# Optimization experiments

Measured on AMD Instinct MI355X. Metric: run time of the kernel, lower is better.

## Reference

```python
import jax, jax.numpy as jnp
import numpy as np

B, T, FEA, H, OUT, L = 40, 20, 200, 1024, 1095, 12


def setup_inputs() -> dict:
    key = jax.random.key(0)
    ks = jax.random.split(key, 8)

    def init(k, shape, fan_in):
        return jax.random.normal(k, shape, jnp.float32) * (1.0 / np.sqrt(fan_in))

    return {
        "x": jax.random.normal(ks[0], (B, T, FEA), jnp.float32),
        "hidden": jnp.zeros((L, B, H), jnp.float32),  # initial SRU cell state c0 per layer
        "W1": init(ks[1], (FEA, H), FEA),
        "b1": jnp.zeros((H,), jnp.float32),
        "sru_W": init(ks[2], (L, H, 3 * H), H),   # per layer: [x_tilde | f-gate | r-gate]
        "sru_b": jnp.zeros((L, 2 * H), jnp.float32),  # per layer: [b_f | b_r]
        "W3": init(ks[3], (H, H), H),
        "b3": jnp.zeros((H,), jnp.float32),
        "W4": init(ks[4], (H, OUT), H),
        "b4": jnp.zeros((OUT,), jnp.float32),
    }


def _sru_layer(x, c0, W, b):
    # x: [t, b, h]; SRU (Lei et al. 2017) with use_tanh=True and highway on x
    U = jnp.einsum('tbh,hk->tbk', x, W)          # [t, b, 3h]
    x_tilde, uf, ur = jnp.split(U, 3, axis=-1)
    bf, br = jnp.split(b, 2)
    f = jax.nn.sigmoid(uf + bf)                  # forget gate
    r = jax.nn.sigmoid(ur + br)                  # reset/highway gate

    def step(c, ins):
        ft, xt = ins
        c = ft * c + (1.0 - ft) * xt
        return c, c

    c_last, cs = jax.lax.scan(step, c0, (f, x_tilde))
    h = r * jnp.tanh(cs) + (1.0 - r) * x
    return h, c_last


def reference(x, hidden, W1, b1, sru_W, sru_b, W3, b3, W4, b4):
    b, t, _ = x.shape
    # Dense_layer1 (dropout is identity at inference)
    h = jnp.dot(x.reshape(b * t, -1), W1) + b1
    h = h.reshape(b, t, H).transpose(1, 0, 2)    # [t, b, H] (time-major for SRU)
    c_finals = []
    for l in range(sru_W.shape[0]):
        h, c_l = _sru_layer(h, hidden[l], sru_W[l], sru_b[l])
        c_finals.append(c_l)
    hidden_after = jnp.stack(c_finals)           # [L, b, H]
    h = h.transpose(1, 0, 2).reshape(b * t, H)
    h = jax.nn.relu(jnp.dot(h, W3) + b3)
    out = jnp.dot(h, W4) + b4                    # [b*t, OUT]
    return out, hidden_after
```

## Files before the change

kernel.cpp:

```cpp
#include <hip/hip_runtime.h>
#include <hip/hip_bf16.h>
#include <math.h>

typedef __bf16 bf16_t;
typedef __bf16 bf16x8 __attribute__((ext_vector_type(8)));
typedef float f32x4 __attribute__((ext_vector_type(4)));
typedef unsigned short u16;

#define NB   40
#define NT   20
#define FEA  200
#define HD   1024
#define NOUT 1095
#define NL   12
#define M_ROWS 800
#define UPITCH 196

#define FBUF 36864
#define GBUF 24576

__global__ __launch_bounds__(256)
void transpose_convert(const float* __restrict__ src, bf16_t* __restrict__ dst,
                       int srcK, int srcN, int Kp, int Np)
{
    __shared__ u16 tile[64 * 66];
    const int t = threadIdx.x;
    src += (size_t)blockIdx.z * srcK * srcN;
    dst += (size_t)blockIdx.z * Np * Kp;
    const int n0 = blockIdx.x << 6, k0 = blockIdx.y << 6;
    {
        const int nl = t & 63, kb = (t >> 6) << 4;
        const int gn = n0 + nl;
        #pragma unroll
        for (int j = 0; j < 16; j++) {
            const int gk = k0 + kb + j;
            float v = (gk < srcK && gn < srcN) ? src[(size_t)gk * srcN + gn] : 0.f;
            bf16_t b = (bf16_t)v;
            tile[nl * 66 + kb + j] = *(const u16*)&b;
        }
    }
    __syncthreads();
    {
        const int nl = t >> 2, kg = (t & 3) << 4;
        const unsigned* tp = (const unsigned*)tile;
        const int dw = nl * 33 + (kg >> 1);
        uint4 v0, v1;
        v0.x = tp[dw+0]; v0.y = tp[dw+1]; v0.z = tp[dw+2]; v0.w = tp[dw+3];
        v1.x = tp[dw+4]; v1.y = tp[dw+5]; v1.z = tp[dw+6]; v1.w = tp[dw+7];
        bf16_t* dp = dst + (size_t)(n0 + nl) * Kp + k0 + kg;
        *(uint4*)dp = v0;
        *(uint4*)(dp + 8) = v1;
    }
}

__global__ __launch_bounds__(256)
void convert_pad_x(const float* __restrict__ src, bf16_t* __restrict__ dst)
{
    const int m = blockIdx.x, k = threadIdx.x;
    dst[m * 256 + k] = (bf16_t)((k < FEA) ? src[(size_t)m * FEA + k] : 0.f);
}

template<bool OUT_F32, bool RELU>
__global__ __launch_bounds__(256)
void gemm_tiled(const bf16_t* __restrict__ A, const bf16_t* __restrict__ Bt,
                const float* __restrict__ bias, void* __restrict__ C,
                int M, int Nstore, int Ks)
{
    extern __shared__ char lds[];
    const int tid = threadIdx.x;
    const int w = tid >> 6, lane = tid & 63, quad = lane >> 4, l16 = lane & 15;
    const int n0 = blockIdx.x << 6;
    const int m0 = blockIdx.y << 7;
    const int wr = w >> 1, wc = w & 1;

    const int lrow  = lane >> 3;
    const int gslot = ((lane & 7) ^ lrow) << 3;
    const bf16_t* aSrc[4];
    const bf16_t* bSrc[2];
    #pragma unroll
    for (int i = 0; i < 4; i++) {
        int r = m0 + (w * 4 + i) * 8 + lrow;
        if (r > M - 1) r = M - 1;
        aSrc[i] = A + (size_t)r * Ks + gslot;
    }
    #pragma unroll
    for (int i = 0; i < 2; i++)
        bSrc[i] = Bt + (size_t)(n0 + (w * 2 + i) * 8 + lrow) * Ks + gslot;

    f32x4 acc[4][2];
    #pragma unroll
    for (int m = 0; m < 4; m++)
        #pragma unroll
        for (int n = 0; n < 2; n++) acc[m][n] = (f32x4){0.f, 0.f, 0.f, 0.f};

    const int nkt = Ks >> 6;

    #define STAGE(kt) do {                                                     \
        const int _k0 = (kt) << 6;                                             \
        char* _b = lds + ((kt) & 3) * GBUF;                                    \
        _Pragma("unroll")                                                      \
        for (int _i = 0; _i < 4; _i++)                                         \
            __builtin_amdgcn_global_load_lds(                                  \
                (const __attribute__((address_space(1))) void*)(aSrc[_i] + _k0),\
                (__attribute__((address_space(3))) void*)(_b + (w * 4 + _i) * 1024), \
                16, 0, 0);                                                     \
        _Pragma("unroll")                                                      \
        for (int _i = 0; _i < 2; _i++)                                         \
            __builtin_amdgcn_global_load_lds(                                  \
                (const __attribute__((address_space(1))) void*)(bSrc[_i] + _k0),\
                (__attribute__((address_space(3))) void*)(_b + 16384 + (w * 2 + _i) * 1024), \
                16, 0, 0);                                                     \
    } while (0)

    STAGE(0);
    if (nkt > 1) STAGE(1);

    for (int kt = 0; kt < nkt; kt++) {
        if (kt + 2 < nkt) STAGE(kt + 2);
        const int rem = nkt - 1 - kt;
        if (rem >= 2)      asm volatile("s_waitcnt vmcnt(12)" ::: "memory");
        else if (rem == 1) asm volatile("s_waitcnt vmcnt(6)"  ::: "memory");
        else               asm volatile("s_waitcnt vmcnt(0)"  ::: "memory");
        __builtin_amdgcn_s_barrier();

        const char* ab = lds + (kt & 3) * GBUF;
        #pragma unroll
        for (int kk = 0; kk < 2; kk++) {
            const int ts = (kk << 2) + quad;
            bf16x8 a[4], b[2];
            #pragma unroll
            for (int m = 0; m < 4; m++) {
                const int r = wr * 64 + m * 16 + l16;
                a[m] = *(const bf16x8*)(ab + r * 128 + ((ts ^ (r & 7)) << 4));
            }
            #pragma unroll
            for (int n = 0; n < 2; n++) {
                const int r = wc * 32 + n * 16 + l16;
                b[n] = *(const bf16x8*)(ab + 16384 + r * 128 + ((ts ^ (r & 7)) << 4));
            }
            #pragma unroll
            for (int m = 0; m < 4; m++)
                #pragma unroll
                for (int n = 0; n < 2; n++)
                    acc[m][n] = __builtin_amdgcn_mfma_f32_16x16x32_bf16(a[m], b[n], acc[m][n], 0, 0, 0);
        }
    }
    #undef STAGE

    #pragma unroll
    for (int n = 0; n < 2; n++) {
        const int col = n0 + wc * 32 + n * 16 + l16;
        if (col >= Nstore) continue;
        const float bv = bias ? bias[col] : 0.f;
        #pragma unroll
        for (int m = 0; m < 4; m++) {
            #pragma unroll
            for (int i = 0; i < 4; i++) {
                const int mg = m0 + wr * 64 + m * 16 + quad * 4 + i;
                if (mg < M) {
                    float v = acc[m][n][i] + bv;
                    if (RELU) v = v > 0.f ? v : 0.f;
                    if (OUT_F32) ((float*)C)[(size_t)mg * Nstore + col] = v;
                    else         ((bf16_t*)C)[(size_t)mg * Nstore + col] = (bf16_t)v;
                }
            }
        }
    }
}

__global__ __launch_bounds__(256)
void sru_layer_fused(const bf16_t* __restrict__ hin, bf16_t* __restrict__ hout,
                     const bf16_t* __restrict__ Wt, const float* __restrict__ c0,
                     const float* __restrict__ bvec, float* __restrict__ cout)
{
    extern __shared__ char lds_raw[];
    const int tid = threadIdx.x;
    const int w = tid >> 6, lane = tid & 63, quad = lane >> 4, l16 = lane & 15;
    const int n0 = blockIdx.x << 6;
    const int m0 = blockIdx.y * 80;

    const int lrow  = lane >> 3;
    const int gslot = ((lane & 7) ^ lrow) << 3;

    const bf16_t* aSrc[3];
    #pragma unroll
    for (int i = 0; i < 3; i++) {
        int r = (w * 3 + i) * 8 + lrow;
        if (r > 79) r = 79;
        aSrc[i] = hin + (size_t)(m0 + r) * HD + gslot;
    }
    const bf16_t* bSrc[6];
    #pragma unroll
    for (int i = 0; i < 6; i++) {
        const int r = (w * 6 + i) * 8 + lrow;
        bSrc[i] = Wt + (size_t)((r >> 6) * HD + n0 + (r & 63)) * HD + gslot;
    }

    f32x4 acc[5][3];
    #pragma unroll
    for (int m = 0; m < 5; m++)
        #pragma unroll
        for (int n = 0; n < 3; n++) acc[m][n] = (f32x4){0.f, 0.f, 0.f, 0.f};

    #define STAGEF(kt) do {                                                    \
        const int _k0 = (kt) << 6;                                             \
        char* _b = lds_raw + ((kt) & 3) * FBUF;                                \
        _Pragma("unroll")                                                      \
        for (int _i = 0; _i < 3; _i++)                                         \
            __builtin_amdgcn_global_load_lds(                                  \
                (const __attribute__((address_space(1))) void*)(aSrc[_i] + _k0), \
                (__attribute__((address_space(3))) void*)(_b + (w * 3 + _i) * 1024), \
                16, 0, 0);                                                     \
        _Pragma("unroll")                                                      \
        for (int _i = 0; _i < 6; _i++)                                         \
            __builtin_amdgcn_global_load_lds(                                  \
                (const __attribute__((address_space(1))) void*)(bSrc[_i] + _k0), \
                (__attribute__((address_space(3))) void*)(_b + 12288 + (w * 6 + _i) * 1024), \
                16, 0, 0);                                                     \
    } while (0)

    STAGEF(0);
    STAGEF(1);

    for (int kt = 0; kt < 16; kt++) {
        if (kt + 2 < 16) STAGEF(kt + 2);
        const int rem = 15 - kt;
        if (rem >= 2)      asm volatile("s_waitcnt vmcnt(18)" ::: "memory");
        else if (rem == 1) asm volatile("s_waitcnt vmcnt(9)"  ::: "memory");
        else               asm volatile("s_waitcnt vmcnt(0)"  ::: "memory");
        __builtin_amdgcn_s_barrier();

        const char* ab = lds_raw + (kt & 3) * FBUF;
        const char* bb = ab + 12288;
        #pragma unroll
        for (int kk = 0; kk < 2; kk++) {
            const int ts = (kk << 2) + quad;
            bf16x8 a[5], b[3];
            #pragma unroll
            for (int m = 0; m < 5; m++) {
                const int r = m * 16 + l16;
                a[m] = *(const bf16x8*)(ab + r * 128 + ((ts ^ (r & 7)) << 4));
            }
            #pragma unroll
            for (int n = 0; n < 3; n++) {
                const int r = (w * 3 + n) * 16 + l16;
                b[n] = *(const bf16x8*)(bb + r * 128 + ((ts ^ (r & 7)) << 4));
            }
            #pragma unroll
            for (int m = 0; m < 5; m++)
                #pragma unroll
                for (int n = 0; n < 3; n++)
                    acc[m][n] = __builtin_amdgcn_mfma_f32_16x16x32_bf16(a[m], b[n], acc[m][n], 0, 0, 0);
        }
    }
    #undef STAGEF

    float* Ul = (float*)lds_raw;
    #pragma unroll
    for (int m = 0; m < 5; m++)
        #pragma unroll
        for (int n = 0; n < 3; n++) {
            const int col = (w * 3 + n) * 16 + l16;
            #pragma unroll
            for (int i = 0; i < 4; i++)
                Ul[(m * 16 + quad * 4 + i) * UPITCH + col] = acc[m][n][i];
        }
    __syncthreads();

    const int bl = tid >> 6, nn = tid & 63, bg = blockIdx.y * 4 + bl;
    float c = c0[(size_t)bg * HD + n0 + nn];
    const float bfb = bvec[n0 + nn], brb = bvec[HD + n0 + nn];
    for (int t = 0; t < NT; t++) {
        const float* u = &Ul[(bl * NT + t) * UPITCH];
        const float xt = u[nn];
        const float uf = u[64 + nn];
        const float ur = u[128 + nn];
        const float f = 1.f / (1.f + __expf(-(uf + bfb)));
        const float r = 1.f / (1.f + __expf(-(ur + brb)));
        c = f * c + (1.f - f) * xt;
        const size_t gi = (size_t)(bg * NT + t) * HD + n0 + nn;
        const float hp = (float)hin[gi];
        hout[gi] = (bf16_t)(r * tanhf(c) + (1.f - r) * hp);
    }
    cout[(size_t)bg * HD + n0 + nn] = c;
}

extern "C" void kernel_launch(void* const* d_in, const int* in_sizes, int n_in,
                              void* d_out, int out_size, void* d_ws, size_t ws_size,
                              hipStream_t stream)
{
    const float* x      = (const float*)d_in[0];
    const float* hidden = (const float*)d_in[1];
    const float* W1     = (const float*)d_in[2];
    const float* b1     = (const float*)d_in[3];
    const float* sruW   = (const float*)d_in[4];
    const float* srub   = (const float*)d_in[5];
    const float* W3     = (const float*)d_in[6];
    const float* b3     = (const float*)d_in[7];
    const float* W4     = (const float*)d_in[8];
    const float* b4     = (const float*)d_in[9];

    float* out     = (float*)d_out;
    float* hid_out = out + (size_t)M_ROWS * NOUT;

    bf16_t* h0 = (bf16_t*)d_out;

    hipFuncSetAttribute((const void*)sru_layer_fused,
                        hipFuncAttributeMaxDynamicSharedMemorySize, 4 * FBUF);
    hipFuncSetAttribute((const void*)gemm_tiled<false, false>,
                        hipFuncAttributeMaxDynamicSharedMemorySize, 4 * GBUF);
    hipFuncSetAttribute((const void*)gemm_tiled<false, true>,
                        hipFuncAttributeMaxDynamicSharedMemorySize, 4 * GBUF);
    hipFuncSetAttribute((const void*)gemm_tiled<true, false>,
                        hipFuncAttributeMaxDynamicSharedMemorySize, 4 * GBUF);

    char* ws = (char*)d_ws;
    const size_t SZ_WT  = (size_t)NL * 3 * HD * HD * 2;
    const size_t SZ_W1  = (size_t)HD * 256 * 2;
    const size_t SZ_W3  = (size_t)HD * HD * 2;
    const size_t SZ_W4  = (size_t)1152 * HD * 2;
    const size_t SZ_XB  = (size_t)M_ROWS * 256 * 2;
    const size_t SZ_H   = (size_t)M_ROWS * HD * 2;
    const size_t SLOT   = (size_t)3 * HD * HD * 2;
    const size_t FAST_NEED = SZ_WT + SZ_W1 + SZ_W3 + SZ_W4 + SZ_XB + 2 * SZ_H;
    const bool fast = ws_size >= FAST_NEED;

    const dim3 blk(256);
    const int GY = (M_ROWS + 127) >> 7;

    if (fast) {
        bf16_t* wt  = (bf16_t*)ws;
        bf16_t* w1t = (bf16_t*)(ws + SZ_WT);
        bf16_t* w3t = (bf16_t*)(ws + SZ_WT + SZ_W1);
        bf16_t* w4t = (bf16_t*)(ws + SZ_WT + SZ_W1 + SZ_W3);
        bf16_t* xb  = (bf16_t*)(ws + SZ_WT + SZ_W1 + SZ_W3 + SZ_W4);
        bf16_t* h1  = (bf16_t*)(ws + SZ_WT + SZ_W1 + SZ_W3 + SZ_W4 + SZ_XB);
        bf16_t* g   = (bf16_t*)(ws + SZ_WT + SZ_W1 + SZ_W3 + SZ_W4 + SZ_XB + SZ_H);

        convert_pad_x<<<M_ROWS, blk, 0, stream>>>(x, xb);
        transpose_convert<<<dim3(16, 4, 1),  blk, 0, stream>>>(W1,   w1t, FEA, HD,    256, HD);
        transpose_convert<<<dim3(48, 16, NL), blk, 0, stream>>>(sruW, wt,  HD,  3*HD, HD,  3*HD);
        transpose_convert<<<dim3(16, 16, 1), blk, 0, stream>>>(W3,   w3t, HD,  HD,   HD,  HD);
        transpose_convert<<<dim3(18, 16, 1), blk, 0, stream>>>(W4,   w4t, HD,  NOUT, HD,  1152);

        gemm_tiled<false, false><<<dim3(16, GY), blk, 4 * GBUF, stream>>>(xb, w1t, b1, h0, M_ROWS, HD, 256);

        for (int l = 0; l < NL; l++) {
            const bf16_t* hi = (l & 1) ? h1 : h0;
            bf16_t*       ho = (l & 1) ? h0 : h1;
            sru_layer_fused<<<dim3(16, 10), blk, 4 * FBUF, stream>>>(
                hi, ho, wt + (size_t)l * 3 * HD * HD,
                hidden + (size_t)l * NB * HD, srub + (size_t)l * 2 * HD,
                hid_out + (size_t)l * NB * HD);
        }
        gemm_tiled<false, true><<<dim3(16, GY), blk, 4 * GBUF, stream>>>(h0, w3t, b3, g, M_ROWS, HD, HD);
        gemm_tiled<true, false><<<dim3(18, GY), blk, 4 * GBUF, stream>>>(g, w4t, b4, out, M_ROWS, NOUT, HD);
    } else {
        bf16_t* slot = (bf16_t*)ws;
        bf16_t* xb   = (bf16_t*)(ws + SLOT);
        bf16_t* h1   = (bf16_t*)(ws + SLOT + SZ_XB);
        bf16_t* g    = (bf16_t*)(ws + SLOT + SZ_XB + SZ_H);

        convert_pad_x<<<M_ROWS, blk, 0, stream>>>(x, xb);
        transpose_convert<<<dim3(16, 4, 1), blk, 0, stream>>>(W1, slot, FEA, HD, 256, HD);
        gemm_tiled<false, false><<<dim3(16, GY), blk, 4 * GBUF, stream>>>(xb, slot, b1, h0, M_ROWS, HD, 256);

        for (int l = 0; l < NL; l++) {
            transpose_convert<<<dim3(48, 16, 1), blk, 0, stream>>>(
                sruW + (size_t)l * HD * 3 * HD, slot, HD, 3*HD, HD, 3*HD);
            const bf16_t* hi = (l & 1) ? h1 : h0;
            bf16_t*       ho = (l & 1) ? h0 : h1;
            sru_layer_fused<<<dim3(16, 10), blk, 4 * FBUF, stream>>>(
                hi, ho, slot,
                hidden + (size_t)l * NB * HD, srub + (size_t)l * 2 * HD,
                hid_out + (size_t)l * NB * HD);
        }
        transpose_convert<<<dim3(16, 16, 1), blk, 0, stream>>>(W3, slot, HD, HD, HD, HD);
        gemm_tiled<false, true><<<dim3(16, GY), blk, 4 * GBUF, stream>>>(h0, slot, b3, g, M_ROWS, HD, HD);
        transpose_convert<<<dim3(18, 16, 1), blk, 0, stream>>>(W4, slot, HD, NOUT, HD, 1152);
        gemm_tiled<true, false><<<dim3(18, GY), blk, 4 * GBUF, stream>>>(g, slot, b4, out, M_ROWS, NOUT, HD);
    }
}
```

Measured before the change: 544.5 us.

## Prefetch next layer weights into L2, vectorize transpose loads, fast tanh

```diff
diff --git a/kernel.cpp b/kernel.cpp
--- a/kernel.cpp
+++ b/kernel.cpp
@@ -28,7 +28,29 @@
     src += (size_t)blockIdx.z * srcK * srcN;
     dst += (size_t)blockIdx.z * Np * Kp;
     const int n0 = blockIdx.x << 6, k0 = blockIdx.y << 6;
-    {
+
+    if ((srcN & 3) == 0) {
+        const int nc4 = (t & 15) << 2, kr = t >> 4;
+        const int gn = n0 + nc4;
+        #pragma unroll
+        for (int j = 0; j < 4; j++) {
+            const int gk = k0 + kr + j * 16;
+            float4 v = {0.f, 0.f, 0.f, 0.f};
+            if (gk < srcK && gn + 3 < srcN)
+                v = *(const float4*)(src + (size_t)gk * srcN + gn);
+            else if (gk < srcK) {
+                float* vp = (float*)&v;
+                for (int c = 0; c < 4; c++)
+                    if (gn + c < srcN) vp[c] = src[(size_t)gk * srcN + gn + c];
+            }
+            const float* vp = (const float*)&v;
+            #pragma unroll
+            for (int c = 0; c < 4; c++) {
+                bf16_t b = (bf16_t)vp[c];
+                tile[(nc4 + c) * 66 + kr + j * 16] = *(const u16*)&b;
+            }
+        }
+    } else {
         const int nl = t & 63, kb = (t >> 6) << 4;
         const int gn = n0 + nl;
         #pragma unroll
@@ -60,11 +82,33 @@
     dst[m * 256 + k] = (bf16_t)((k < FEA) ? src[(size_t)m * FEA + k] : 0.f);
 }
 
+__device__ __forceinline__
+void l2_prefetch(const bf16_t* pfwt, int pfnc, int n0, int tid)
+{
+    if (pfnc <= 0) return;
+    unsigned pv[12];
+    #pragma unroll
+    for (int g = 0; g < 3; g++) {
+        if (g < pfnc) {
+            const char* base = (const char*)(pfwt + (size_t)(g * HD + n0) * HD);
+            #pragma unroll
+            for (int q = 0; q < 4; q++)
+                pv[g * 4 + q] = *(const unsigned*)(base + (size_t)(q * 256 + tid) * 128);
+        } else {
+            #pragma unroll
+            for (int q = 0; q < 4; q++) pv[g * 4 + q] = 0u;
+        }
+    }
+    #pragma unroll
+    for (int i = 0; i < 12; i++) asm volatile("" :: "v"(pv[i]));
+}
+
 template<bool OUT_F32, bool RELU>
 __global__ __launch_bounds__(256)
 void gemm_tiled(const bf16_t* __restrict__ A, const bf16_t* __restrict__ Bt,
                 const float* __restrict__ bias, void* __restrict__ C,
-                int M, int Nstore, int Ks)
+                int M, int Nstore, int Ks,
+                const bf16_t* __restrict__ pfwt, int pfnc)
 {
     extern __shared__ char lds[];
     const int tid = threadIdx.x;
@@ -147,6 +191,8 @@
     }
     #undef STAGE
 
+    l2_prefetch(pfwt, pfnc, n0, tid);
+
     #pragma unroll
     for (int n = 0; n < 2; n++) {
         const int col = n0 + wc * 32 + n * 16 + l16;
@@ -171,7 +217,8 @@
 __global__ __launch_bounds__(256)
 void sru_layer_fused(const bf16_t* __restrict__ hin, bf16_t* __restrict__ hout,
                      const bf16_t* __restrict__ Wt, const float* __restrict__ c0,
-                     const float* __restrict__ bvec, float* __restrict__ cout)
+                     const float* __restrict__ bvec, float* __restrict__ cout,
+                     const bf16_t* __restrict__ pfwt, int pfnc)
 {
     extern __shared__ char lds_raw[];
     const int tid = threadIdx.x;
@@ -192,8 +239,8 @@
     const bf16_t* bSrc[6];
     #pragma unroll
     for (int i = 0; i < 6; i++) {
-        const int r = (w * 6 + i) * 8 + lrow;
-        bSrc[i] = Wt + (size_t)((r >> 6) * HD + n0 + (r & 63)) * HD + gslot;
+        const int rb = (w * 6 + i) * 8 + lrow;
+        bSrc[i] = Wt + (size_t)((rb >> 6) * HD + n0 + (rb & 63)) * HD + gslot;
     }
 
     f32x4 acc[5][3];
@@ -255,6 +302,8 @@
     }
     #undef STAGEF
 
+    __syncthreads();
+
     float* Ul = (float*)lds_raw;
     #pragma unroll
     for (int m = 0; m < 5; m++)
@@ -270,6 +319,7 @@
     const int bl = tid >> 6, nn = tid & 63, bg = blockIdx.y * 4 + bl;
     float c = c0[(size_t)bg * HD + n0 + nn];
     const float bfb = bvec[n0 + nn], brb = bvec[HD + n0 + nn];
+    #pragma unroll
     for (int t = 0; t < NT; t++) {
         const float* u = &Ul[(bl * NT + t) * UPITCH];
         const float xt = u[nn];
@@ -278,10 +328,16 @@
         const float f = 1.f / (1.f + __expf(-(uf + bfb)));
         const float r = 1.f / (1.f + __expf(-(ur + brb)));
         c = f * c + (1.f - f) * xt;
+        const float e  = __expf(-2.f * fabsf(c));
+        float th = (1.f - e) / (1.f + e);
+        th = (c < 0.f) ? -th : th;
         const size_t gi = (size_t)(bg * NT + t) * HD + n0 + nn;
         const float hp = (float)hin[gi];
-        hout[gi] = (bf16_t)(r * tanhf(c) + (1.f - r) * hp);
-    }
+        hout[gi] = (bf16_t)(r * th + (1.f - r) * hp);
+    }
+
+    l2_prefetch(pfwt, pfnc, n0, tid);
+
     cout[(size_t)bg * HD + n0 + nn] = c;
 }
 
@@ -343,18 +399,23 @@
         transpose_convert<<<dim3(16, 16, 1), blk, 0, stream>>>(W3,   w3t, HD,  HD,   HD,  HD);
         transpose_convert<<<dim3(18, 16, 1), blk, 0, stream>>>(W4,   w4t, HD,  NOUT, HD,  1152);
 
-        gemm_tiled<false, false><<<dim3(16, GY), blk, 4 * GBUF, stream>>>(xb, w1t, b1, h0, M_ROWS, HD, 256);
+        gemm_tiled<false, false><<<dim3(16, GY), blk, 4 * GBUF, stream>>>(
+            xb, w1t, b1, h0, M_ROWS, HD, 256, wt, 3);
 
         for (int l = 0; l < NL; l++) {
             const bf16_t* hi = (l & 1) ? h1 : h0;
             bf16_t*       ho = (l & 1) ? h0 : h1;
+            const bf16_t* pfw = (l + 1 < NL) ? wt + (size_t)(l + 1) * 3 * HD * HD : w3t;
+            const int     pfn = (l + 1 < NL) ? 3 : 1;
             sru_layer_fused<<<dim3(16, 10), blk, 4 * FBUF, stream>>>(
                 hi, ho, wt + (size_t)l * 3 * HD * HD,
                 hidden + (size_t)l * NB * HD, srub + (size_t)l * 2 * HD,
-                hid_out + (size_t)l * NB * HD);
-        }
-        gemm_tiled<false, true><<<dim3(16, GY), blk, 4 * GBUF, stream>>>(h0, w3t, b3, g, M_ROWS, HD, HD);
-        gemm_tiled<true, false><<<dim3(18, GY), blk, 4 * GBUF, stream>>>(g, w4t, b4, out, M_ROWS, NOUT, HD);
+                hid_out + (size_t)l * NB * HD, pfw, pfn);
+        }
+        gemm_tiled<false, true><<<dim3(16, GY), blk, 4 * GBUF, stream>>>(
+            h0, w3t, b3, g, M_ROWS, HD, HD, w4t, 1);
+        gemm_tiled<true, false><<<dim3(18, GY), blk, 4 * GBUF, stream>>>(
+            g, w4t, b4, out, M_ROWS, NOUT, HD, (const bf16_t*)0, 0);
     } else {
         bf16_t* slot = (bf16_t*)ws;
         bf16_t* xb   = (bf16_t*)(ws + SLOT);
@@ -363,7 +424,8 @@
 
         convert_pad_x<<<M_ROWS, blk, 0, stream>>>(x, xb);
         transpose_convert<<<dim3(16, 4, 1), blk, 0, stream>>>(W1, slot, FEA, HD, 256, HD);
-        gemm_tiled<false, false><<<dim3(16, GY), blk, 4 * GBUF, stream>>>(xb, slot, b1, h0, M_ROWS, HD, 256);
+        gemm_tiled<false, false><<<dim3(16, GY), blk, 4 * GBUF, stream>>>(
+            xb, slot, b1, h0, M_ROWS, HD, 256, (const bf16_t*)0, 0);
 
         for (int l = 0; l < NL; l++) {
             transpose_convert<<<dim3(48, 16, 1), blk, 0, stream>>>(
@@ -373,11 +435,13 @@
             sru_layer_fused<<<dim3(16, 10), blk, 4 * FBUF, stream>>>(
                 hi, ho, slot,
                 hidden + (size_t)l * NB * HD, srub + (size_t)l * 2 * HD,
-                hid_out + (size_t)l * NB * HD);
+                hid_out + (size_t)l * NB * HD, (const bf16_t*)0, 0);
         }
         transpose_convert<<<dim3(16, 16, 1), blk, 0, stream>>>(W3, slot, HD, HD, HD, HD);
-        gemm_tiled<false, true><<<dim3(16, GY), blk, 4 * GBUF, stream>>>(h0, slot, b3, g, M_ROWS, HD, HD);
+        gemm_tiled<false, true><<<dim3(16, GY), blk, 4 * GBUF, stream>>>(
+            h0, slot, b3, g, M_ROWS, HD, HD, (const bf16_t*)0, 0);
         transpose_convert<<<dim3(18, 16, 1), blk, 0, stream>>>(W4, slot, HD, NOUT, HD, 1152);
-        gemm_tiled<true, false><<<dim3(18, GY), blk, 4 * GBUF, stream>>>(g, slot, b4, out, M_ROWS, NOUT, HD);
-    }
-}
+        gemm_tiled<true, false><<<dim3(18, GY), blk, 4 * GBUF, stream>>>(
+            g, slot, b4, out, M_ROWS, NOUT, HD, (const bf16_t*)0, 0);
+    }
+}
```

Result: no change. 537.6 us (-1.3%).
